# Kernel tuning notes

Hardware: AMD Instinct MI355X
Metric: run time of the kernel (lower is better)

## Reference

```python
import jax, jax.numpy as jnp
import numpy as np

VOCAB = 90000
MAX_ID = 95000
EFFECT_DIM = 758
ADD_DIM = 10
EMBED_DIM = 768  # EFFECT_DIM + ADD_DIM
CTX = 1024
MAX_SYN = 8


def setup_inputs() -> dict:
    key = jax.random.key(0)
    k_ids, k_emb, k_rev, k_tab, k_msk = jax.random.split(key, 5)
    ids = jax.random.randint(k_ids, (CTX,), 0, VOCAB, dtype=jnp.int64)
    W_emb = jax.random.normal(k_emb, (MAX_ID, EFFECT_DIM), dtype=jnp.float32)
    W_rev = jax.random.normal(k_rev, (EMBED_DIM, MAX_ID), dtype=jnp.float32)
    padding = 0.1 * jnp.ones((CTX, ADD_DIM), dtype=jnp.float32)
    # synonym ids live in [VOCAB, MAX_ID); only some slots are active (variable-length lists)
    syn_table = jax.random.randint(k_tab, (MAX_ID, MAX_SYN), VOCAB, MAX_ID, dtype=jnp.int32)
    syn_mask = jax.random.randint(k_msk, (MAX_ID, MAX_SYN), 0, 2, dtype=jnp.int32)
    # tokens >= VOCAB (synonym ids themselves) have no synonyms
    syn_mask = syn_mask.at[VOCAB:].set(0)
    return {"ids": ids, "W_emb": W_emb, "W_rev": W_rev, "padding": padding,
            "syn_table": syn_table, "syn_mask": syn_mask}


def reference(ids, W_emb, W_rev, padding, syn_table, syn_mask):
    # VirtualEmbedding: base gather + masked synonym gather/scale/accumulate.
    # i_sum is computed BEFORE the synonym loop in the original, so each
    # synonym contribution is independent -> vectorized masked reduction.
    # (Dropout in eval mode is the identity.)
    base = W_emb[ids]                              # [L, D]
    syn_ids = syn_table[ids]                       # [L, K]
    syn = W_emb[syn_ids]                           # [L, K, D]
    mask = syn_mask[ids].astype(base.dtype)        # [L, K]
    i_sum = jnp.sum(base, axis=-1, keepdims=True)  # [L, 1]
    s_sum = jnp.sum(syn, axis=-1)                  # [L, K]
    d = i_sum / s_sum                              # [L, K]
    emb = base + jnp.einsum('lk,lkd->ld', mask * d, syn)
    # concat fixed context padding, then ReverseEmbedding projection to vocab
    full = jnp.concatenate([emb, padding], axis=1)  # [L, EMBED_DIM]
    return full @ W_rev                             # [L, MAX_ID]
```

## Files before the change

kernel.cpp:

```cpp
#include <hip/hip_runtime.h>
#include <stdint.h>

#define EFFECT_DIM 758
#define ADD_DIM 10
#define EMBED_DIM 768
#define NCOLS 95000
#define NSYN 8
#define NROWS 1024
#define NT256 372
#define TILE_B 32768

typedef __attribute__((ext_vector_type(8))) __bf16 bf16x8;
typedef __attribute__((ext_vector_type(16))) float f32x16;
typedef __attribute__((ext_vector_type(4))) uint32_t u32x4;


static __device__ __forceinline__ uint32_t pack2(float a, float b) {
  uint32_t r;
  asm("v_cvt_pk_bf16_f32 %0, %1, %2" : "=v"(r) : "v"(a), "v"(b));
  return r;
}

#define GLOAD16(src, dst)                                                   \
  __builtin_amdgcn_global_load_lds(                                         \
      (const __attribute__((address_space(1))) uint32_t*)(src),             \
      (__attribute__((address_space(3))) uint32_t*)(dst), 16, 0, 0)

#define F4C(f, i) ((i) == 0 ? (f).x : (i) == 1 ? (f).y : (i) == 2 ? (f).z : (f).w)

__global__ __launch_bounds__(256) void emb_kernel(
    const int* __restrict__ ids, const float* __restrict__ W_emb,
    const float* __restrict__ padding, const int* __restrict__ syn_table,
    const int* __restrict__ syn_mask, char* __restrict__ ws)
{
  const int l = blockIdx.x;
  const int t = threadIdx.x;
  const int id = ids[l];
  int sid[NSYN];
  int msk[NSYN];
#pragma unroll
  for (int k = 0; k < NSYN; ++k) {
    sid[k] = syn_table[id * NSYN + k];
    msk[k] = syn_mask[id * NSYN + k];
  }

  double p[9] = {0, 0, 0, 0, 0, 0, 0, 0, 0};
  for (int d = t; d < EFFECT_DIM; d += 256) {
    p[0] += (double)W_emb[(size_t)id * EFFECT_DIM + d];
#pragma unroll
    for (int k = 0; k < NSYN; ++k)
      p[k + 1] += (double)W_emb[(size_t)sid[k] * EFFECT_DIM + d];
  }

  __shared__ double s_red[9][4];
  const int w = t >> 6;
#pragma unroll
  for (int k = 0; k < 9; ++k) {
    double v = p[k];
#pragma unroll
    for (int off = 32; off > 0; off >>= 1) v += __shfl_down(v, off, 64);
    if ((t & 63) == 0) s_red[k][w] = v;
  }
  __syncthreads();

  const double isum = s_red[0][0] + s_red[0][1] + s_red[0][2] + s_red[0][3];
  float coef[NSYN];
#pragma unroll
  for (int k = 0; k < NSYN; ++k) {
    double ss = s_red[k + 1][0] + s_red[k + 1][1] + s_red[k + 1][2] + s_red[k + 1][3];
    coef[k] = msk[k] ? (float)(isum / ss) : 0.0f;
  }

  const int r = l & 255;
  char* wbase = ws + (size_t)(l >> 8) * (12 * TILE_B);

  for (int j = t; j < 384; j += 256) {
    const int d0 = 2 * j;
    float v0, v1;
    if (d0 < EFFECT_DIM) {
      const float* bp = W_emb + (size_t)id * EFFECT_DIM + d0;
      v0 = bp[0];
      v1 = bp[1];
#pragma unroll
      for (int k = 0; k < NSYN; ++k) {
        const float* sp = W_emb + (size_t)sid[k] * EFFECT_DIM + d0;
        v0 = fmaf(coef[k], sp[0], v0);
        v1 = fmaf(coef[k], sp[1], v1);
      }
    } else {
      v0 = padding[l * ADD_DIM + (d0 - EFFECT_DIM)];
      v1 = padding[l * ADD_DIM + (d0 + 1 - EFFECT_DIM)];
    }
    const int ks   = j >> 5;
    const int jl   = j & 31;
    const int kk   = jl >> 3;
    const int byte = (jl & 7) * 4;
    const int lane = (r & 31) + ((byte >> 4) << 5);
    *(uint32_t*)(wbase + ks * TILE_B + kk * 8192 + (r >> 5) * 1024 +
                 lane * 16 + (byte & 15)) = pack2(v0, v1);
  }
}

__global__ __launch_bounds__(256) void conv_kernel(
    const float* __restrict__ Wrev, char* __restrict__ Bbuf)
{
  __shared__ char lds[16384];
  const int t   = threadIdx.x;
  const int j   = blockIdx.x;
  const int ks  = blockIdx.y;
  const int nl4 = t & 31;
  const int kc  = t >> 5;
  const int gn4 = j * 128 + nl4 * 4;
  const bool valid = (gn4 + 4) <= NCOLS;

  float4 v[8];
  const float* p = Wrev + (size_t)(ks * 64 + kc * 8) * NCOLS + gn4;
#pragma unroll
  for (int jj = 0; jj < 8; ++jj)
    v[jj] = valid ? *(const float4*)(p + (size_t)jj * NCOLS)
                  : float4{0.0f, 0.0f, 0.0f, 0.0f};

  const int kk  = kc >> 1;
  const int lh2 = kc & 1;
#pragma unroll
  for (int i = 0; i < 4; ++i) {
    const int nloc = nl4 * 4 + i;
    u32x4 u;
#pragma unroll
    for (int j2 = 0; j2 < 4; ++j2)
      u[j2] = pack2(F4C(v[2 * j2], i), F4C(v[2 * j2 + 1], i));
    const int lane = (nloc & 31) + (lh2 << 5);
    *(u32x4*)(lds + kk * 4096 + (nl4 >> 3) * 1024 + lane * 16) = u;
  }
  __syncthreads();

  char* base = Bbuf + (size_t)((j >> 1) * 12 + ks) * TILE_B + (j & 1) * 4096;
#pragma unroll
  for (int i = 0; i < 4; ++i) {
    const int idx = i * 4096 + t * 16;
    const int k2  = idx >> 12;
    const int rem = idx & 4095;
    *(u32x4*)(base + k2 * 8192 + rem) = *(const u32x4*)(lds + idx);
  }
}

__global__ __launch_bounds__(512, 2) void gemm_pre(
    const char* __restrict__ Abuf, const char* __restrict__ Bbuf,
    float* __restrict__ out)
{
  extern __shared__ char lds[];
  const int t = threadIdx.x;
  const int l = t & 63;
  const int w = t >> 6;
  const int wm = w >> 2;
  const int wn = w & 3;

  const int wgid = blockIdx.x;
  const int xcd  = wgid & 7;
  const int work = xcd * 186 + (wgid >> 3);
  const int mt = work & 3;
  const int nt = work >> 2;
  const int n0 = nt * 256;

  const char* asrc = Abuf + (size_t)mt * (12 * TILE_B);
  const char* bsrc = Bbuf + (size_t)nt * (12 * TILE_B);
  const int soff = t * 16;
  const int doff = w * 1024;

#define STAGEU(s, ksi, kkk)                                                  \
  {                                                                          \
    GLOAD16(asrc + (ksi)*TILE_B + (kkk)*8192 + soff,                         \
            lds + (s)*65536 + (kkk)*8192 + doff);                            \
    GLOAD16(bsrc + (ksi)*TILE_B + (kkk)*8192 + soff,                         \
            lds + (s)*65536 + 32768 + (kkk)*8192 + doff);                    \
  }

#pragma unroll
  for (int kk = 0; kk < 4; ++kk) STAGEU(0, 0, kk);

  f32x16 acc[4][2] = {};

  for (int T = 0; T < 12; ++T) {
    const int cs = T & 1;
    const char* aw = lds + cs * 65536 + (wm * 4) * 1024 + l * 16;
    const char* bw = lds + cs * 65536 + 32768 + (wn * 2) * 1024 + l * 16;
    const int Tn = (T < 11) ? T + 1 : 11;

#pragma unroll
    for (int p = 0; p < 4; ++p) {
      STAGEU(cs ^ 1, Tn, p);
      asm volatile("s_waitcnt vmcnt(8)" ::: "memory");
      __builtin_amdgcn_sched_barrier(0);
      __builtin_amdgcn_s_barrier();

      bf16x8 a[4], b[2];
#pragma unroll
      for (int mr = 0; mr < 4; ++mr)
        a[mr] = *(const bf16x8*)(aw + p * 8192 + mr * 1024);
#pragma unroll
      for (int nr = 0; nr < 2; ++nr)
        b[nr] = *(const bf16x8*)(bw + p * 8192 + nr * 1024);

      __builtin_amdgcn_s_setprio(1);
#pragma unroll
      for (int mr = 0; mr < 4; ++mr)
#pragma unroll
        for (int nr = 0; nr < 2; ++nr)
          acc[mr][nr] = __builtin_amdgcn_mfma_f32_32x32x16_bf16(
              a[mr], b[nr], acc[mr][nr], 0, 0, 0);
      __builtin_amdgcn_s_setprio(0);
    }
  }
#undef STAGEU

  asm volatile("s_waitcnt vmcnt(0)" ::: "memory");

  const int lh = l >> 5;
#pragma unroll
  for (int nr = 0; nr < 2; ++nr) {
    const int gc = n0 + wn * 64 + nr * 32 + (l & 31);
    if (gc < NCOLS) {
#pragma unroll
      for (int mr = 0; mr < 4; ++mr)
#pragma unroll
        for (int reg = 0; reg < 16; ++reg) {
          const int row = mt * 256 + wm * 128 + mr * 32 +
                          (reg & 3) + 8 * (reg >> 2) + 4 * lh;
          out[(size_t)row * NCOLS + gc] = acc[mr][nr][reg];
        }
    }
  }
}

extern "C" void kernel_launch(void* const* d_in, const int* in_sizes, int n_in,
                              void* d_out, int out_size, void* d_ws, size_t ws_size,
                              hipStream_t stream) {
  const int*   ids       = (const int*)d_in[0];
  const float* W_emb     = (const float*)d_in[1];
  const float* W_rev     = (const float*)d_in[2];
  const float* padding   = (const float*)d_in[3];
  const int*   syn_table = (const int*)d_in[4];
  const int*   syn_mask  = (const int*)d_in[5];
  float* out = (float*)d_out;
  char*  ws  = (char*)d_ws;

  const size_t A_BYTES = (size_t)4 * 12 * TILE_B;
  const size_t B_BYTES = (size_t)NT256 * 12 * TILE_B;

  hipLaunchKernelGGL(emb_kernel, dim3(NROWS), dim3(256), 0, stream,
                     ids, W_emb, padding, syn_table, syn_mask, ws);

  if (ws_size >= A_BYTES + B_BYTES) {
    char* Bbuf = ws + A_BYTES;
    hipLaunchKernelGGL(conv_kernel, dim3(NT256 * 2, 12), dim3(256), 0, stream,
                       W_rev, Bbuf);
    hipLaunchKernelGGL(gemm_pre, dim3(4 * NT256), dim3(512), 131072, stream,
                       ws, Bbuf, out);
  } else {
    hipLaunchKernelGGL(gemm_pre, dim3(4 * NT256), dim3(512), 131072, stream,
                       ws, ws, out);
  }
}
```

Baseline: 369.3 us.

## Fuse W_rev bf16 conversion into GEMM main loop, dropping conv kernel

Removes the separate kernel that converted W_rev to a tiled bf16 buffer. The GEMM now loads fp32 W_rev columns straight into registers, packs them to bf16 and writes the swizzled tile into LDS for the next stage. This avoids writing the bf16 copy of W_rev and reading it back, and drops one launch. It also moves to one barrier per K-stage instead of one per sub-step. In exchange, each M-tile block re-reads fp32 B, relying on L2 sharing between neighbouring blocks, and adds 32 registers of B data per thread plus VALU pack work inside the GEMM.

```diff
diff --git a/kernel.cpp b/kernel.cpp
--- a/kernel.cpp
+++ b/kernel.cpp
@@ -25,8 +25,6 @@
   __builtin_amdgcn_global_load_lds(                                         \
       (const __attribute__((address_space(1))) uint32_t*)(src),             \
       (__attribute__((address_space(3))) uint32_t*)(dst), 16, 0, 0)
-
-#define F4C(f, i) ((i) == 0 ? (f).x : (i) == 1 ? (f).y : (i) == 2 ? (f).z : (f).w)
 
 __global__ __launch_bounds__(256) void emb_kernel(
     const int* __restrict__ ids, const float* __restrict__ W_emb,
@@ -101,51 +99,8 @@
   }
 }
 
-__global__ __launch_bounds__(256) void conv_kernel(
-    const float* __restrict__ Wrev, char* __restrict__ Bbuf)
-{
-  __shared__ char lds[16384];
-  const int t   = threadIdx.x;
-  const int j   = blockIdx.x;
-  const int ks  = blockIdx.y;
-  const int nl4 = t & 31;
-  const int kc  = t >> 5;
-  const int gn4 = j * 128 + nl4 * 4;
-  const bool valid = (gn4 + 4) <= NCOLS;
-
-  float4 v[8];
-  const float* p = Wrev + (size_t)(ks * 64 + kc * 8) * NCOLS + gn4;
-#pragma unroll
-  for (int jj = 0; jj < 8; ++jj)
-    v[jj] = valid ? *(const float4*)(p + (size_t)jj * NCOLS)
-                  : float4{0.0f, 0.0f, 0.0f, 0.0f};
-
-  const int kk  = kc >> 1;
-  const int lh2 = kc & 1;
-#pragma unroll
-  for (int i = 0; i < 4; ++i) {
-    const int nloc = nl4 * 4 + i;
-    u32x4 u;
-#pragma unroll
-    for (int j2 = 0; j2 < 4; ++j2)
-      u[j2] = pack2(F4C(v[2 * j2], i), F4C(v[2 * j2 + 1], i));
-    const int lane = (nloc & 31) + (lh2 << 5);
-    *(u32x4*)(lds + kk * 4096 + (nl4 >> 3) * 1024 + lane * 16) = u;
-  }
-  __syncthreads();
-
-  char* base = Bbuf + (size_t)((j >> 1) * 12 + ks) * TILE_B + (j & 1) * 4096;
-#pragma unroll
-  for (int i = 0; i < 4; ++i) {
-    const int idx = i * 4096 + t * 16;
-    const int k2  = idx >> 12;
-    const int rem = idx & 4095;
-    *(u32x4*)(base + k2 * 8192 + rem) = *(const u32x4*)(lds + idx);
-  }
-}
-
-__global__ __launch_bounds__(512, 2) void gemm_pre(
-    const char* __restrict__ Abuf, const char* __restrict__ Bbuf,
+__global__ __launch_bounds__(512, 2) void gemm_fused(
+    const float* __restrict__ Wrev, const char* __restrict__ Abuf,
     float* __restrict__ out)
 {
   extern __shared__ char lds[];
@@ -163,36 +118,64 @@
   const int n0 = nt * 256;
 
   const char* asrc = Abuf + (size_t)mt * (12 * TILE_B);
-  const char* bsrc = Bbuf + (size_t)nt * (12 * TILE_B);
-  const int soff = t * 16;
-  const int doff = w * 1024;
-
-#define STAGEU(s, ksi, kkk)                                                  \
+
+  const int sn = t & 255;
+  const int kg = t >> 8;
+  const int gn = n0 + sn;
+  const bool valid = gn < NCOLS;
+
+  float br[32];
+
+#define AGLD(s, ksi)                                                         \
   {                                                                          \
-    GLOAD16(asrc + (ksi)*TILE_B + (kkk)*8192 + soff,                         \
-            lds + (s)*65536 + (kkk)*8192 + doff);                            \
-    GLOAD16(bsrc + (ksi)*TILE_B + (kkk)*8192 + soff,                         \
-            lds + (s)*65536 + 32768 + (kkk)*8192 + doff);                    \
-  }
-
-#pragma unroll
-  for (int kk = 0; kk < 4; ++kk) STAGEU(0, 0, kk);
+    _Pragma("unroll") for (int kk = 0; kk < 4; ++kk)                         \
+      GLOAD16(asrc + (ksi)*TILE_B + kk*8192 + t*16,                          \
+              lds + (s)*65536 + kk*8192 + w*1024);                           \
+  }
+
+#define BLOAD(ksi)                                                           \
+  {                                                                          \
+    const float* p = Wrev + (size_t)((ksi)*64 + kg*32) * NCOLS + gn;         \
+    _Pragma("unroll") for (int j = 0; j < 32; ++j)                           \
+      br[j] = valid ? p[(size_t)j * NCOLS] : 0.0f;                           \
+  }
+
+#define BSTORE(s)                                                            \
+  {                                                                          \
+    _Pragma("unroll") for (int c = 0; c < 2; ++c) {                          \
+      u32x4 u0, u1;                                                          \
+      _Pragma("unroll") for (int j = 0; j < 4; ++j) {                        \
+        u0[j] = pack2(br[c*16 + 2*j],     br[c*16 + 2*j + 1]);               \
+        u1[j] = pack2(br[c*16 + 8 + 2*j], br[c*16 + 9 + 2*j]);               \
+      }                                                                      \
+      char* bb = lds + (s)*65536 + 32768 + (kg*2 + c)*8192 + (sn>>5)*1024;   \
+      *(u32x4*)(bb + (sn & 31)*16) = u0;                                     \
+      *(u32x4*)(bb + ((sn & 31) + 32)*16) = u1;                              \
+    }                                                                        \
+  }
+
+  AGLD(0, 0);
+  BLOAD(0);
+  BSTORE(0);
+  asm volatile("s_waitcnt vmcnt(0) lgkmcnt(0)" ::: "memory");
+  __builtin_amdgcn_s_barrier();
 
   f32x16 acc[4][2] = {};
 
   for (int T = 0; T < 12; ++T) {
     const int cs = T & 1;
+    const int Tn = (T < 11) ? T + 1 : 11;
+
+    __builtin_amdgcn_sched_barrier(0);
+    AGLD(cs ^ 1, Tn);
+    BLOAD(Tn);
+    __builtin_amdgcn_sched_barrier(0);
+
     const char* aw = lds + cs * 65536 + (wm * 4) * 1024 + l * 16;
     const char* bw = lds + cs * 65536 + 32768 + (wn * 2) * 1024 + l * 16;
-    const int Tn = (T < 11) ? T + 1 : 11;
 
 #pragma unroll
     for (int p = 0; p < 4; ++p) {
-      STAGEU(cs ^ 1, Tn, p);
-      asm volatile("s_waitcnt vmcnt(8)" ::: "memory");
-      __builtin_amdgcn_sched_barrier(0);
-      __builtin_amdgcn_s_barrier();
-
       bf16x8 a[4], b[2];
 #pragma unroll
       for (int mr = 0; mr < 4; ++mr)
@@ -200,7 +183,6 @@
 #pragma unroll
       for (int nr = 0; nr < 2; ++nr)
         b[nr] = *(const bf16x8*)(bw + p * 8192 + nr * 1024);
-
       __builtin_amdgcn_s_setprio(1);
 #pragma unroll
       for (int mr = 0; mr < 4; ++mr)
@@ -210,10 +192,16 @@
               a[mr], b[nr], acc[mr][nr], 0, 0, 0);
       __builtin_amdgcn_s_setprio(0);
     }
-  }
-#undef STAGEU
-
-  asm volatile("s_waitcnt vmcnt(0)" ::: "memory");
+
+    __builtin_amdgcn_sched_barrier(0);
+    BSTORE(cs ^ 1);
+    asm volatile("s_waitcnt lgkmcnt(0)" ::: "memory");
+    __builtin_amdgcn_sched_barrier(0);
+    __builtin_amdgcn_s_barrier();
+  }
+#undef AGLD
+#undef BLOAD
+#undef BSTORE
 
   const int lh = l >> 5;
 #pragma unroll
@@ -244,20 +232,9 @@
   float* out = (float*)d_out;
   char*  ws  = (char*)d_ws;
 
-  const size_t A_BYTES = (size_t)4 * 12 * TILE_B;
-  const size_t B_BYTES = (size_t)NT256 * 12 * TILE_B;
-
   hipLaunchKernelGGL(emb_kernel, dim3(NROWS), dim3(256), 0, stream,
                      ids, W_emb, padding, syn_table, syn_mask, ws);
 
-  if (ws_size >= A_BYTES + B_BYTES) {
-    char* Bbuf = ws + A_BYTES;
-    hipLaunchKernelGGL(conv_kernel, dim3(NT256 * 2, 12), dim3(256), 0, stream,
-                       W_rev, Bbuf);
-    hipLaunchKernelGGL(gemm_pre, dim3(4 * NT256), dim3(512), 131072, stream,
-                       ws, Bbuf, out);
-  } else {
-    hipLaunchKernelGGL(gemm_pre, dim3(4 * NT256), dim3(512), 131072, stream,
-                       ws, ws, out);
-  }
-}
+  hipLaunchKernelGGL(gemm_fused, dim3(4 * NT256), dim3(512), 131072, stream,
+                     W_rev, ws, out);
+}
```

Result: faster. 343.4 us (-7.0%).
